# Kernel optimization log

Measured on AMD Instinct MI355X. Metric: run time of the kernel, lower is better.

The kernel has to match this reference:

```python
import jax, jax.numpy as jnp
import numpy as np

D_MODEL = 1024
N_HEADS = 16
D_K = D_MODEL // N_HEADS


def setup_inputs() -> dict:
    key = jax.random.key(0)
    ks = jax.random.split(key, 10)
    s = 1.0 / np.sqrt(D_MODEL)
    def lin(k):
        kw, kb = jax.random.split(k)
        W = jax.random.uniform(kw, (D_MODEL, D_MODEL), jnp.float32, -s, s)
        b = jax.random.uniform(kb, (D_MODEL,), jnp.float32, -s, s)
        return W, b
    Wq, bq = lin(ks[0])
    Wk, bk = lin(ks[1])
    Wv, bv = lin(ks[2])
    Wo, bo = lin(ks[3])
    x = jax.random.normal(ks[4], (2, 2048, D_MODEL), jnp.float32)
    gamma = jnp.ones((D_MODEL,), jnp.float32)
    beta = jnp.zeros((D_MODEL,), jnp.float32)
    return {"x": x, "Wq": Wq, "bq": bq, "Wk": Wk, "bk": bk,
            "Wv": Wv, "bv": bv, "Wo": Wo, "bo": bo,
            "gamma": gamma, "beta": beta}


def _mha(x, Wq, bq, Wk, bk, Wv, bv, Wo, bo, gamma, beta):
    B, S, _ = x.shape
    residual = x
    # Linear uses y = x @ W.T + b (torch nn.Linear convention)
    q = (x @ Wq.T + bq).reshape(B, S, N_HEADS, D_K).transpose(0, 2, 1, 3)
    k = (x @ Wk.T + bk).reshape(B, S, N_HEADS, D_K).transpose(0, 2, 1, 3)
    v = (x @ Wv.T + bv).reshape(B, S, N_HEADS, D_K).transpose(0, 2, 1, 3)
    scores = jnp.einsum("bhqd,bhkd->bhqk", q, k) / jnp.sqrt(jnp.float32(D_K))
    attn = jax.nn.softmax(scores, axis=-1)
    out = jnp.einsum("bhqk,bhkd->bhqd", attn, v)
    out = out.transpose(0, 2, 1, 3).reshape(B, S, D_MODEL)
    out = out @ Wo.T + bo
    h = out + residual
    mu = jnp.mean(h, axis=-1, keepdims=True)
    var = jnp.var(h, axis=-1, keepdims=True)
    h = (h - mu) / jnp.sqrt(var + 1e-5) * gamma + beta
    return jnp.where(h >= 0, h, 0.01 * h)


def reference(x, Wq, bq, Wk, bk, Wv, bv, Wo, bo, gamma, beta):
    return _mha(x, Wq, bq, Wk, bk, Wv, bv, Wo, bo, gamma, beta)
```

## Files before the change

### kernel.cpp

```cpp
#include <hip/hip_runtime.h>

#define DM   1024
#define NH   16
#define DK   64
#define SEQ  2048
#define BATCH 2

typedef __attribute__((ext_vector_type(8))) short bf16x8;
typedef __attribute__((ext_vector_type(4))) float f32x4;
typedef __attribute__((ext_vector_type(16))) float f32x16;

__device__ __forceinline__ unsigned short f2bf(float f) {
    unsigned int u = __builtin_bit_cast(unsigned int, f);
    u += 0x7FFFu + ((u >> 16) & 1u);
    return (unsigned short)(u >> 16);
}

__global__ __launch_bounds__(256)
void cvt_kernel(const float* __restrict__ x,
                const float* __restrict__ wq, const float* __restrict__ wk,
                const float* __restrict__ wv, const float* __restrict__ wo,
                unsigned short* __restrict__ xb,
                unsigned short* __restrict__ wqkvb,
                unsigned short* __restrict__ wob)
{
    const int seg = blockIdx.y;
    const float* src;
    unsigned short* dst;
    int n;
    if (seg == 0)      { src = x;  dst = xb;                  n = 4 << 20; }
    else if (seg == 1) { src = wq; dst = wqkvb;               n = 1 << 20; }
    else if (seg == 2) { src = wk; dst = wqkvb + (1 << 20);   n = 1 << 20; }
    else if (seg == 3) { src = wv; dst = wqkvb + (2 << 20);   n = 1 << 20; }
    else               { src = wo; dst = wob;                 n = 1 << 20; }
    for (int i = (blockIdx.x * 256 + threadIdx.x) * 4; i < n; i += 1024 * 256 * 4) {
        const float4 v = *reinterpret_cast<const float4*>(&src[i]);
        ushort4 o;
        o.x = f2bf(v.x); o.y = f2bf(v.y); o.z = f2bf(v.z); o.w = f2bf(v.w);
        *reinterpret_cast<ushort4*>(&dst[i]) = o;
    }
}

template <int MODE, int BN>
__global__ __launch_bounds__(256)
void gemm2_kernel(const unsigned short* __restrict__ Ab,
                  const unsigned short* __restrict__ Wall,
                  const float* __restrict__ B0, const float* __restrict__ B1,
                  const float* __restrict__ B2,
                  unsigned short* __restrict__ q_ws,
                  unsigned short* __restrict__ k_ws,
                  unsigned short* __restrict__ vt_ws,
                  const float* __restrict__ resid,
                  float* __restrict__ h_ws)
{
    __shared__ unsigned short sA[128 * 32];
    __shared__ unsigned short sB[BN * 32];

    const int tid = threadIdx.x, lane = tid & 63, wid = tid >> 6;
    const int n0 = blockIdx.x * BN, m0 = blockIdx.y * 128;
    const int z  = (MODE == 0) ? blockIdx.z : 0;
    const unsigned short* W = Wall + (size_t)z * (1 << 20);
    const float* bias = (MODE == 0) ? (z == 0 ? B0 : (z == 1 ? B1 : B2)) : B0;

    const int g = lane >> 4, lq = lane & 15;
    const int wr = wid >> 1, wc = wid & 1;
    const int rA = lane >> 2;
    const int csh = (lane & 3) * 8;

    f32x4 acc[4][BN / 32] = {};

    for (int k0 = 0; k0 < DM; k0 += 32) {
        #pragma unroll
        for (int i = 0; i < 2; ++i) {
            const int c = wid * 2 + i;
            __builtin_amdgcn_global_load_lds(
                (const __attribute__((address_space(1))) unsigned int*)
                    &Ab[(size_t)(m0 + c * 16 + rA) * DM + k0 + csh],
                (__attribute__((address_space(3))) unsigned int*)&sA[c * 512],
                16, 0, 0);
        }
        #pragma unroll
        for (int i = 0; i < BN / 64; ++i) {
            const int c = wid * (BN / 64) + i;
            __builtin_amdgcn_global_load_lds(
                (const __attribute__((address_space(1))) unsigned int*)
                    &W[(size_t)(n0 + c * 16 + rA) * DM + k0 + csh],
                (__attribute__((address_space(3))) unsigned int*)&sB[c * 512],
                16, 0, 0);
        }
        __syncthreads();

        bf16x8 a[4], b[BN / 32];
        #pragma unroll
        for (int m = 0; m < 4; ++m)
            a[m] = *reinterpret_cast<const bf16x8*>(&sA[(wr * 64 + m * 16 + lq) * 32 + 8 * g]);
        #pragma unroll
        for (int n = 0; n < BN / 32; ++n)
            b[n] = *reinterpret_cast<const bf16x8*>(&sB[(wc * (BN / 2) + n * 16 + lq) * 32 + 8 * g]);
        #pragma unroll
        for (int m = 0; m < 4; ++m)
            #pragma unroll
            for (int n = 0; n < BN / 32; ++n)
                acc[m][n] = __builtin_amdgcn_mfma_f32_16x16x32_bf16(
                    a[m], b[n], acc[m][n], 0, 0, 0);
        __syncthreads();
    }

    #pragma unroll
    for (int m = 0; m < 4; ++m) {
        #pragma unroll
        for (int n = 0; n < BN / 32; ++n) {
            #pragma unroll
            for (int j = 0; j < 4; ++j) {
                const int row = m0 + wr * 64 + m * 16 + 4 * g + j;
                const int col = n0 + wc * (BN / 2) + n * 16 + lq;
                float v = acc[m][n][j] + bias[col];
                if constexpr (MODE == 0) {
                    const int b_ = row >> 11, s = row & (SEQ - 1);
                    const int hh = col >> 6,  d = col & (DK - 1);
                    if (z == 0)
                        q_ws[(((size_t)(b_ * NH + hh) * SEQ + s) << 6) + d] = f2bf(v * 0.18033688f);
                    else if (z == 1)
                        k_ws[(((size_t)(b_ * NH + hh) * SEQ + s) << 6) + d] = f2bf(v);
                    else
                        vt_ws[((size_t)(b_ * NH + hh) * DK + d) * SEQ + s] = f2bf(v);
                } else {
                    const size_t idx = (size_t)row * DM + col;
                    h_ws[idx] = v + resid[idx];
                }
            }
        }
    }
}

__global__ __launch_bounds__(512)
void attn_kernel(const unsigned short* __restrict__ q_ws,
                 const unsigned short* __restrict__ k_ws,
                 const unsigned short* __restrict__ vt_ws,
                 unsigned short* __restrict__ ao_ws)
{
    __shared__ unsigned short lds4[8][4096];

    const int tid = threadIdx.x;
    const int lane = tid & 63, wid = tid >> 6;
    const int s = wid >> 2, w4 = wid & 3;
    const int l31 = lane & 31, h = lane >> 5;

    const int bid  = blockIdx.x + 16 * blockIdx.y;
    const int xcd  = bid & 7, slot = bid >> 3;
    const int bh   = 4 * xcd + (slot >> 4);
    const int q0   = (slot & 15) * 128;
    const int q    = q0 + w4 * 32 + l31;

    const size_t qbase = ((size_t)bh * SEQ + q) * DK;
    bf16x8 qf[4];
    #pragma unroll
    for (int j = 0; j < 4; ++j)
        qf[j] = *reinterpret_cast<const bf16x8*>(&q_ws[qbase + j * 16 + h * 8]);

    const short one_bf = (short)0x3F80;
    const bf16x8 onesf = {one_bf, one_bf, one_bf, one_bf, one_bf, one_bf, one_bf, one_bf};

    const int l8 = lane >> 3, l7 = lane & 7;
    const int scol = 8 * (l7 ^ l8);
    const unsigned short* kp0 = &k_ws [((size_t)bh * SEQ + s * 1024 + w4 * 16 + l8) * DK + scol];
    const unsigned short* kp1 = kp0 + 8 * DK;
    const unsigned short* vp0 = &vt_ws[((size_t)bh * DK + w4 * 16 + l8) * SEQ + s * 1024 + scol];
    const unsigned short* vp1 = vp0 + 8 * SEQ;

    const int r7 = l31 & 7;
    const unsigned short* pK[4];
    const unsigned short* pV[4];
    #pragma unroll
    for (int j = 0; j < 4; ++j) {
        const int ck = 8 * (((j << 1) + h) ^ r7);
        pK[j] = &lds4[2 * s][l31 * 64 + ck];
        pV[j] = &lds4[4 + 2 * s][l31 * 64 + ck];
    }

    f32x16 oacc[2] = {};
    f32x16 lacc = {};

    const int dst0 = w4 * 2 * 512, dst1 = (w4 * 2 + 1) * 512;

    auto stage = [&](int b) {
        __builtin_amdgcn_global_load_lds(
            (const __attribute__((address_space(1))) unsigned int*)kp0,
            (__attribute__((address_space(3))) unsigned int*)&lds4[2 * s + b][dst0], 16, 0, 0);
        __builtin_amdgcn_global_load_lds(
            (const __attribute__((address_space(1))) unsigned int*)kp1,
            (__attribute__((address_space(3))) unsigned int*)&lds4[2 * s + b][dst1], 16, 0, 0);
        __builtin_amdgcn_global_load_lds(
            (const __attribute__((address_space(1))) unsigned int*)vp0,
            (__attribute__((address_space(3))) unsigned int*)&lds4[4 + 2 * s + b][dst0], 16, 0, 0);
        __builtin_amdgcn_global_load_lds(
            (const __attribute__((address_space(1))) unsigned int*)vp1,
            (__attribute__((address_space(3))) unsigned int*)&lds4[4 + 2 * s + b][dst1], 16, 0, 0);
        kp0 += 64 * DK; kp1 += 64 * DK;
        vp0 += 64;      vp1 += 64;
    };

    auto compute = [&](int OFF) {
        f32x16 st0 = {}, st1 = {};
        __builtin_amdgcn_s_setprio(1);
        #pragma unroll
        for (int j = 0; j < 4; ++j) {
            const bf16x8 k0 = *reinterpret_cast<const bf16x8*>(pK[j] + OFF);
            const bf16x8 k1 = *reinterpret_cast<const bf16x8*>(pK[j] + OFF + 2048);
            st0 = __builtin_amdgcn_mfma_f32_32x32x16_bf16(k0, qf[j], st0, 0, 0, 0);
            st1 = __builtin_amdgcn_mfma_f32_32x32x16_bf16(k1, qf[j], st1, 0, 0, 0);
        }
        __builtin_amdgcn_s_setprio(0);

        bf16x8 pb[4];
        #pragma unroll
        for (int ss = 0; ss < 2; ++ss) {
            #pragma unroll
            for (int jg = 0; jg < 2; ++jg) {
                const int rb = 8 * jg;
                float e0, e1, e2, e3, e4, e5, e6, e7;
                #define EXP2(dst, src) asm("v_exp_f32 %0, %1" : "=v"(dst) : "v"(src))
                if (ss == 0) {
                    EXP2(e0, st0[rb + 0]); EXP2(e1, st0[rb + 1]);
                    EXP2(e2, st0[rb + 2]); EXP2(e3, st0[rb + 3]);
                    EXP2(e4, st0[rb + 4]); EXP2(e5, st0[rb + 5]);
                    EXP2(e6, st0[rb + 6]); EXP2(e7, st0[rb + 7]);
                } else {
                    EXP2(e0, st1[rb + 0]); EXP2(e1, st1[rb + 1]);
                    EXP2(e2, st1[rb + 2]); EXP2(e3, st1[rb + 3]);
                    EXP2(e4, st1[rb + 4]); EXP2(e5, st1[rb + 5]);
                    EXP2(e6, st1[rb + 6]); EXP2(e7, st1[rb + 7]);
                }
                #undef EXP2
                unsigned int wA, wB, wC, wD;
                asm("v_cvt_pk_bf16_f32 %0, %1, %2" : "=v"(wA) : "v"(e0), "v"(e1));
                asm("v_cvt_pk_bf16_f32 %0, %1, %2" : "=v"(wB) : "v"(e2), "v"(e3));
                asm("v_cvt_pk_bf16_f32 %0, %1, %2" : "=v"(wC) : "v"(e4), "v"(e5));
                asm("v_cvt_pk_bf16_f32 %0, %1, %2" : "=v"(wD) : "v"(e6), "v"(e7));
                asm("v_permlane32_swap_b32 %0, %1" : "+v"(wA), "+v"(wC));
                asm("v_permlane32_swap_b32 %0, %1" : "+v"(wB), "+v"(wD));
                uint4 ww;
                ww.x = wA; ww.y = wB; ww.z = wC; ww.w = wD;
                pb[2 * ss + jg] = __builtin_bit_cast(bf16x8, ww);
            }
        }

        __builtin_amdgcn_s_setprio(1);
        #pragma unroll
        for (int jg = 0; jg < 4; ++jg)
            lacc = __builtin_amdgcn_mfma_f32_32x32x16_bf16(onesf, pb[jg], lacc, 0, 0, 0);
        #pragma unroll
        for (int dt = 0; dt < 2; ++dt)
            #pragma unroll
            for (int jg = 0; jg < 4; ++jg) {
                const bf16x8 vv = *reinterpret_cast<const bf16x8*>(pV[jg] + OFF + dt * 2048);
                oacc[dt] = __builtin_amdgcn_mfma_f32_32x32x16_bf16(vv, pb[jg], oacc[dt], 0, 0, 0);
            }
        __builtin_amdgcn_s_setprio(0);
    };

    stage(0);
    __syncthreads();
    #pragma unroll 1
    for (int tt = 0; tt < 8; ++tt) {
        stage(1);
        compute(0);
        __syncthreads();
        if (tt < 7) stage(0);
        compute(4096);
        __syncthreads();
    }

    float* fl = (float*)&lds4[0][0];
    if (s == 1) {
        float* p = fl + (size_t)(w4 * 64 + lane) * 33;
        #pragma unroll
        for (int dt = 0; dt < 2; ++dt)
            #pragma unroll
            for (int r = 0; r < 16; ++r) p[dt * 16 + r] = oacc[dt][r];
        p[32] = lacc[0];
    }
    __syncthreads();
    if (s == 0) {
        const float* p = fl + (size_t)(w4 * 64 + lane) * 33;
        #pragma unroll
        for (int dt = 0; dt < 2; ++dt)
            #pragma unroll
            for (int r = 0; r < 16; ++r) oacc[dt][r] += p[dt * 16 + r];
        const float rl = 1.0f / (lacc[0] + p[32]);

        const int b_ = bh >> 4, hh = bh & 15;
        unsigned short* aop = &ao_ws[(size_t)(b_ * SEQ + q) * DM + hh * 64];
        #pragma unroll
        for (int dt = 0; dt < 2; ++dt) {
            #pragma unroll
            for (int qd = 0; qd < 4; ++qd) {
                ushort4 o;
                o.x = f2bf(oacc[dt][4 * qd + 0] * rl);
                o.y = f2bf(oacc[dt][4 * qd + 1] * rl);
                o.z = f2bf(oacc[dt][4 * qd + 2] * rl);
                o.w = f2bf(oacc[dt][4 * qd + 3] * rl);
                *reinterpret_cast<ushort4*>(&aop[dt * 32 + 8 * qd + 4 * h]) = o;
            }
        }
    }
}

__global__ __launch_bounds__(256)
void ln_kernel(const float* __restrict__ h, const float* __restrict__ gamma,
               const float* __restrict__ beta, float* __restrict__ out)
{
    __shared__ float s1[4], s2[4];
    const int row = blockIdx.x, tid = threadIdx.x;
    const float4 v = reinterpret_cast<const float4*>(h + (size_t)row * DM)[tid];
    float sum = v.x + v.y + v.z + v.w;
    float sq  = v.x * v.x + v.y * v.y + v.z * v.z + v.w * v.w;
    #pragma unroll
    for (int mk = 1; mk <= 32; mk <<= 1) {
        sum += __shfl_xor(sum, mk);
        sq  += __shfl_xor(sq, mk);
    }
    if ((tid & 63) == 0) { s1[tid >> 6] = sum; s2[tid >> 6] = sq; }
    __syncthreads();
    sum = s1[0] + s1[1] + s1[2] + s1[3];
    sq  = s2[0] + s2[1] + s2[2] + s2[3];
    const float mu = sum * (1.f / DM);
    const float var = sq * (1.f / DM) - mu * mu;
    const float rstd = rsqrtf(var + 1e-5f);
    const float4 gv = reinterpret_cast<const float4*>(gamma)[tid];
    const float4 bv = reinterpret_cast<const float4*>(beta)[tid];
    float4 o;
    o.x = (v.x - mu) * rstd * gv.x + bv.x;
    o.y = (v.y - mu) * rstd * gv.y + bv.y;
    o.z = (v.z - mu) * rstd * gv.z + bv.z;
    o.w = (v.w - mu) * rstd * gv.w + bv.w;
    o.x = o.x >= 0.f ? o.x : 0.01f * o.x;
    o.y = o.y >= 0.f ? o.y : 0.01f * o.y;
    o.z = o.z >= 0.f ? o.z : 0.01f * o.z;
    o.w = o.w >= 0.f ? o.w : 0.01f * o.w;
    reinterpret_cast<float4*>(out + (size_t)row * DM)[tid] = o;
}

extern "C" void kernel_launch(void* const* d_in, const int* in_sizes, int n_in,
                              void* d_out, int out_size, void* d_ws, size_t ws_size,
                              hipStream_t stream)
{
    const float* x     = (const float*)d_in[0];
    const float* Wq    = (const float*)d_in[1];
    const float* bq    = (const float*)d_in[2];
    const float* Wk    = (const float*)d_in[3];
    const float* bk    = (const float*)d_in[4];
    const float* Wv    = (const float*)d_in[5];
    const float* bv    = (const float*)d_in[6];
    const float* Wo    = (const float*)d_in[7];
    const float* bo    = (const float*)d_in[8];
    const float* gamma = (const float*)d_in[9];
    const float* beta  = (const float*)d_in[10];

    char* ws = (char*)d_ws;
    unsigned short* q_ws   = (unsigned short*)(ws);
    unsigned short* k_ws   = (unsigned short*)(ws + (8u << 20));
    unsigned short* vt_ws  = (unsigned short*)(ws + (16u << 20));
    unsigned short* ao_ws  = (unsigned short*)(ws + (24u << 20));
    unsigned short* xb_ws  = (unsigned short*)(ws + (32u << 20));
    unsigned short* wqkv_b = (unsigned short*)(ws + (40u << 20));
    unsigned short* wo_b   = (unsigned short*)(ws + (46u << 20));
    float* h_ws = (float*)ws;

    const dim3 blk(256);
    cvt_kernel<<<dim3(1024, 5), blk, 0, stream>>>(
        x, Wq, Wk, Wv, Wo, xb_ws, wqkv_b, wo_b);
    gemm2_kernel<0, 128><<<dim3(8, 32, 3), blk, 0, stream>>>(
        xb_ws, wqkv_b, bq, bk, bv, q_ws, k_ws, vt_ws, nullptr, nullptr);
    attn_kernel<<<dim3(16, 32), dim3(512), 0, stream>>>(q_ws, k_ws, vt_ws, ao_ws);
    gemm2_kernel<1, 64><<<dim3(16, 32, 1), blk, 0, stream>>>(
        ao_ws, wo_b, bo, nullptr, nullptr, nullptr, nullptr, nullptr, x, h_ws);
    ln_kernel<<<dim3(4096), blk, 0, stream>>>(h_ws, gamma, beta, (float*)d_out);
}
```

Measured before the change: 123.5 us.

## Load K/V fragments directly from global memory instead of staging through LDS

The attention kernel no longer double-buffers K and V^T tiles into shared memory with global_load_lds and block barriers. Each wave now reads its MFMA operand fragments straight from global memory, relying on L2/cache reuse across the four waves that share a tile. LDS shrinks to a small combine buffer, and launch bounds ask for higher occupancy. This removes barrier stalls and LDS traffic, but every wave now issues redundant global loads with no explicit prefetch and depends on latency hiding through occupancy.

```diff
diff --git a/kernel.cpp b/kernel.cpp
--- a/kernel.cpp
+++ b/kernel.cpp
@@ -133,13 +133,13 @@
     }
 }
 
-__global__ __launch_bounds__(512)
+__global__ __launch_bounds__(512, 7)
 void attn_kernel(const unsigned short* __restrict__ q_ws,
                  const unsigned short* __restrict__ k_ws,
                  const unsigned short* __restrict__ vt_ws,
                  unsigned short* __restrict__ ao_ws)
 {
-    __shared__ unsigned short lds4[8][4096];
+    __shared__ float comb[8448];
 
     const int tid = threadIdx.x;
     const int lane = tid & 63, wid = tid >> 6;
@@ -161,52 +161,21 @@
     const short one_bf = (short)0x3F80;
     const bf16x8 onesf = {one_bf, one_bf, one_bf, one_bf, one_bf, one_bf, one_bf, one_bf};
 
-    const int l8 = lane >> 3, l7 = lane & 7;
-    const int scol = 8 * (l7 ^ l8);
-    const unsigned short* kp0 = &k_ws [((size_t)bh * SEQ + s * 1024 + w4 * 16 + l8) * DK + scol];
-    const unsigned short* kp1 = kp0 + 8 * DK;
-    const unsigned short* vp0 = &vt_ws[((size_t)bh * DK + w4 * 16 + l8) * SEQ + s * 1024 + scol];
-    const unsigned short* vp1 = vp0 + 8 * SEQ;
-
-    const int r7 = l31 & 7;
-    const unsigned short* pK[4];
-    const unsigned short* pV[4];
-    #pragma unroll
-    for (int j = 0; j < 4; ++j) {
-        const int ck = 8 * (((j << 1) + h) ^ r7);
-        pK[j] = &lds4[2 * s][l31 * 64 + ck];
-        pV[j] = &lds4[4 + 2 * s][l31 * 64 + ck];
-    }
+    const unsigned short* kp  = &k_ws [((size_t)bh * SEQ + s * 1024 + l31) * DK + 8 * h];
+    const unsigned short* vp0 = &vt_ws[((size_t)bh * DK  + l31) * SEQ + s * 1024 + 8 * h];
+    const unsigned short* vp1 = vp0 + (size_t)32 * SEQ;
 
     f32x16 oacc[2] = {};
     f32x16 lacc = {};
 
-    const int dst0 = w4 * 2 * 512, dst1 = (w4 * 2 + 1) * 512;
-
-    auto stage = [&](int b) {
-        __builtin_amdgcn_global_load_lds(
-            (const __attribute__((address_space(1))) unsigned int*)kp0,
-            (__attribute__((address_space(3))) unsigned int*)&lds4[2 * s + b][dst0], 16, 0, 0);
-        __builtin_amdgcn_global_load_lds(
-            (const __attribute__((address_space(1))) unsigned int*)kp1,
-            (__attribute__((address_space(3))) unsigned int*)&lds4[2 * s + b][dst1], 16, 0, 0);
-        __builtin_amdgcn_global_load_lds(
-            (const __attribute__((address_space(1))) unsigned int*)vp0,
-            (__attribute__((address_space(3))) unsigned int*)&lds4[4 + 2 * s + b][dst0], 16, 0, 0);
-        __builtin_amdgcn_global_load_lds(
-            (const __attribute__((address_space(1))) unsigned int*)vp1,
-            (__attribute__((address_space(3))) unsigned int*)&lds4[4 + 2 * s + b][dst1], 16, 0, 0);
-        kp0 += 64 * DK; kp1 += 64 * DK;
-        vp0 += 64;      vp1 += 64;
-    };
-
-    auto compute = [&](int OFF) {
+    #pragma unroll 1
+    for (int t = 0; t < 16; ++t) {
         f32x16 st0 = {}, st1 = {};
         __builtin_amdgcn_s_setprio(1);
         #pragma unroll
         for (int j = 0; j < 4; ++j) {
-            const bf16x8 k0 = *reinterpret_cast<const bf16x8*>(pK[j] + OFF);
-            const bf16x8 k1 = *reinterpret_cast<const bf16x8*>(pK[j] + OFF + 2048);
+            const bf16x8 k0 = *reinterpret_cast<const bf16x8*>(kp + j * 16);
+            const bf16x8 k1 = *reinterpret_cast<const bf16x8*>(kp + 32 * DK + j * 16);
             st0 = __builtin_amdgcn_mfma_f32_32x32x16_bf16(k0, qf[j], st0, 0, 0, 0);
             st1 = __builtin_amdgcn_mfma_f32_32x32x16_bf16(k1, qf[j], st1, 0, 0, 0);
         }
@@ -250,30 +219,24 @@
         for (int jg = 0; jg < 4; ++jg)
             lacc = __builtin_amdgcn_mfma_f32_32x32x16_bf16(onesf, pb[jg], lacc, 0, 0, 0);
         #pragma unroll
-        for (int dt = 0; dt < 2; ++dt)
-            #pragma unroll
-            for (int jg = 0; jg < 4; ++jg) {
-                const bf16x8 vv = *reinterpret_cast<const bf16x8*>(pV[jg] + OFF + dt * 2048);
-                oacc[dt] = __builtin_amdgcn_mfma_f32_32x32x16_bf16(vv, pb[jg], oacc[dt], 0, 0, 0);
-            }
+        for (int jg = 0; jg < 4; ++jg) {
+            const bf16x8 vv = *reinterpret_cast<const bf16x8*>(vp0 + jg * 16);
+            oacc[0] = __builtin_amdgcn_mfma_f32_32x32x16_bf16(vv, pb[jg], oacc[0], 0, 0, 0);
+        }
+        #pragma unroll
+        for (int jg = 0; jg < 4; ++jg) {
+            const bf16x8 vv = *reinterpret_cast<const bf16x8*>(vp1 + jg * 16);
+            oacc[1] = __builtin_amdgcn_mfma_f32_32x32x16_bf16(vv, pb[jg], oacc[1], 0, 0, 0);
+        }
         __builtin_amdgcn_s_setprio(0);
-    };
-
-    stage(0);
-    __syncthreads();
-    #pragma unroll 1
-    for (int tt = 0; tt < 8; ++tt) {
-        stage(1);
-        compute(0);
-        __syncthreads();
-        if (tt < 7) stage(0);
-        compute(4096);
-        __syncthreads();
-    }
-
-    float* fl = (float*)&lds4[0][0];
+
+        kp  += 64 * DK;
+        vp0 += 64;
+        vp1 += 64;
+    }
+
     if (s == 1) {
-        float* p = fl + (size_t)(w4 * 64 + lane) * 33;
+        float* p = comb + (size_t)(w4 * 64 + lane) * 33;
         #pragma unroll
         for (int dt = 0; dt < 2; ++dt)
             #pragma unroll
@@ -282,7 +245,7 @@
     }
     __syncthreads();
     if (s == 0) {
-        const float* p = fl + (size_t)(w4 * 64 + lane) * 33;
+        const float* p = comb + (size_t)(w4 * 64 + lane) * 33;
         #pragma unroll
         for (int dt = 0; dt < 2; ++dt)
             #pragma unroll
```

New measurement: 481.0 us. 290% more time.

## Split attention KV range across four wave groups and drop the ones-MFMA row sum

Applied to the files above, without the earlier changes.

The attention block grows from 512 to 1024 threads, so four wave groups each handle a quarter of the key sequence instead of two groups handling halves. Double buffering is removed: each group single-buffers K and V in LDS with a sync before and after compute. The softmax denominator is now accumulated as a scalar sum of the exponentials plus a permlane swap, replacing the extra MFMA against a ones vector. The partial outputs are combined through LDS in two phases. This adds parallelism and cuts matrix work, but gives up load/compute overlap and adds synchronisation and register pressure under the 1024-thread launch bound.

```diff
diff --git a/kernel.cpp b/kernel.cpp
--- a/kernel.cpp
+++ b/kernel.cpp
@@ -133,7 +133,7 @@
     }
 }
 
-__global__ __launch_bounds__(512)
+__global__ __launch_bounds__(1024)
 void attn_kernel(const unsigned short* __restrict__ q_ws,
                  const unsigned short* __restrict__ k_ws,
                  const unsigned short* __restrict__ vt_ws,
@@ -158,14 +158,11 @@
     for (int j = 0; j < 4; ++j)
         qf[j] = *reinterpret_cast<const bf16x8*>(&q_ws[qbase + j * 16 + h * 8]);
 
-    const short one_bf = (short)0x3F80;
-    const bf16x8 onesf = {one_bf, one_bf, one_bf, one_bf, one_bf, one_bf, one_bf, one_bf};
-
     const int l8 = lane >> 3, l7 = lane & 7;
     const int scol = 8 * (l7 ^ l8);
-    const unsigned short* kp0 = &k_ws [((size_t)bh * SEQ + s * 1024 + w4 * 16 + l8) * DK + scol];
+    const unsigned short* kp0 = &k_ws [((size_t)bh * SEQ + s * 512 + w4 * 16 + l8) * DK + scol];
     const unsigned short* kp1 = kp0 + 8 * DK;
-    const unsigned short* vp0 = &vt_ws[((size_t)bh * DK + w4 * 16 + l8) * SEQ + s * 1024 + scol];
+    const unsigned short* vp0 = &vt_ws[((size_t)bh * DK + w4 * 16 + l8) * SEQ + s * 512 + scol];
     const unsigned short* vp1 = vp0 + 8 * SEQ;
 
     const int r7 = l31 & 7;
@@ -175,38 +172,38 @@
     for (int j = 0; j < 4; ++j) {
         const int ck = 8 * (((j << 1) + h) ^ r7);
         pK[j] = &lds4[2 * s][l31 * 64 + ck];
-        pV[j] = &lds4[4 + 2 * s][l31 * 64 + ck];
+        pV[j] = &lds4[2 * s + 1][l31 * 64 + ck];
     }
 
     f32x16 oacc[2] = {};
-    f32x16 lacc = {};
+    float lsum = 0.f;
 
     const int dst0 = w4 * 2 * 512, dst1 = (w4 * 2 + 1) * 512;
 
-    auto stage = [&](int b) {
+    auto stage = [&]() {
         __builtin_amdgcn_global_load_lds(
             (const __attribute__((address_space(1))) unsigned int*)kp0,
-            (__attribute__((address_space(3))) unsigned int*)&lds4[2 * s + b][dst0], 16, 0, 0);
+            (__attribute__((address_space(3))) unsigned int*)&lds4[2 * s][dst0], 16, 0, 0);
         __builtin_amdgcn_global_load_lds(
             (const __attribute__((address_space(1))) unsigned int*)kp1,
-            (__attribute__((address_space(3))) unsigned int*)&lds4[2 * s + b][dst1], 16, 0, 0);
+            (__attribute__((address_space(3))) unsigned int*)&lds4[2 * s][dst1], 16, 0, 0);
         __builtin_amdgcn_global_load_lds(
             (const __attribute__((address_space(1))) unsigned int*)vp0,
-            (__attribute__((address_space(3))) unsigned int*)&lds4[4 + 2 * s + b][dst0], 16, 0, 0);
+            (__attribute__((address_space(3))) unsigned int*)&lds4[2 * s + 1][dst0], 16, 0, 0);
         __builtin_amdgcn_global_load_lds(
             (const __attribute__((address_space(1))) unsigned int*)vp1,
-            (__attribute__((address_space(3))) unsigned int*)&lds4[4 + 2 * s + b][dst1], 16, 0, 0);
+            (__attribute__((address_space(3))) unsigned int*)&lds4[2 * s + 1][dst1], 16, 0, 0);
         kp0 += 64 * DK; kp1 += 64 * DK;
         vp0 += 64;      vp1 += 64;
     };
 
-    auto compute = [&](int OFF) {
+    auto compute = [&]() {
         f32x16 st0 = {}, st1 = {};
         __builtin_amdgcn_s_setprio(1);
         #pragma unroll
         for (int j = 0; j < 4; ++j) {
-            const bf16x8 k0 = *reinterpret_cast<const bf16x8*>(pK[j] + OFF);
-            const bf16x8 k1 = *reinterpret_cast<const bf16x8*>(pK[j] + OFF + 2048);
+            const bf16x8 k0 = *reinterpret_cast<const bf16x8*>(pK[j]);
+            const bf16x8 k1 = *reinterpret_cast<const bf16x8*>(pK[j] + 2048);
             st0 = __builtin_amdgcn_mfma_f32_32x32x16_bf16(k0, qf[j], st0, 0, 0, 0);
             st1 = __builtin_amdgcn_mfma_f32_32x32x16_bf16(k1, qf[j], st1, 0, 0, 0);
         }
@@ -232,6 +229,7 @@
                     EXP2(e6, st1[rb + 6]); EXP2(e7, st1[rb + 7]);
                 }
                 #undef EXP2
+                lsum += ((e0 + e1) + (e2 + e3)) + ((e4 + e5) + (e6 + e7));
                 unsigned int wA, wB, wC, wD;
                 asm("v_cvt_pk_bf16_f32 %0, %1, %2" : "=v"(wA) : "v"(e0), "v"(e1));
                 asm("v_cvt_pk_bf16_f32 %0, %1, %2" : "=v"(wB) : "v"(e2), "v"(e3));
@@ -247,48 +245,65 @@
 
         __builtin_amdgcn_s_setprio(1);
         #pragma unroll
-        for (int jg = 0; jg < 4; ++jg)
-            lacc = __builtin_amdgcn_mfma_f32_32x32x16_bf16(onesf, pb[jg], lacc, 0, 0, 0);
-        #pragma unroll
         for (int dt = 0; dt < 2; ++dt)
             #pragma unroll
             for (int jg = 0; jg < 4; ++jg) {
-                const bf16x8 vv = *reinterpret_cast<const bf16x8*>(pV[jg] + OFF + dt * 2048);
+                const bf16x8 vv = *reinterpret_cast<const bf16x8*>(pV[jg] + dt * 2048);
                 oacc[dt] = __builtin_amdgcn_mfma_f32_32x32x16_bf16(vv, pb[jg], oacc[dt], 0, 0, 0);
             }
         __builtin_amdgcn_s_setprio(0);
     };
 
-    stage(0);
-    __syncthreads();
     #pragma unroll 1
-    for (int tt = 0; tt < 8; ++tt) {
-        stage(1);
-        compute(0);
-        __syncthreads();
-        if (tt < 7) stage(0);
-        compute(4096);
-        __syncthreads();
-    }
+    for (int t = 0; t < 8; ++t) {
+        stage();
+        __syncthreads();
+        compute();
+        __syncthreads();
+    }
+
+    unsigned int la = __builtin_bit_cast(unsigned int, lsum);
+    unsigned int lb = la;
+    asm("v_permlane32_swap_b32 %0, %1" : "+v"(la), "+v"(lb));
+    float ltot = lsum + __builtin_bit_cast(float, h ? lb : la);
 
     float* fl = (float*)&lds4[0][0];
-    if (s == 1) {
-        float* p = fl + (size_t)(w4 * 64 + lane) * 33;
-        #pragma unroll
-        for (int dt = 0; dt < 2; ++dt)
-            #pragma unroll
-            for (int r = 0; r < 16; ++r) p[dt * 16 + r] = oacc[dt][r];
-        p[32] = lacc[0];
-    }
-    __syncthreads();
+    {
+        if (s > 0) {
+            float* p = fl + (size_t)((s - 1) * 256 + w4 * 64 + lane) * 17;
+            #pragma unroll
+            for (int r = 0; r < 16; ++r) p[r] = oacc[0][r];
+            p[16] = ltot;
+        }
+        __syncthreads();
+        if (s == 0) {
+            #pragma unroll
+            for (int ss2 = 0; ss2 < 3; ++ss2) {
+                const float* p = fl + (size_t)(ss2 * 256 + w4 * 64 + lane) * 17;
+                #pragma unroll
+                for (int r = 0; r < 16; ++r) oacc[0][r] += p[r];
+                ltot += p[16];
+            }
+        }
+        __syncthreads();
+        if (s > 0) {
+            float* p = fl + (size_t)((s - 1) * 256 + w4 * 64 + lane) * 17;
+            #pragma unroll
+            for (int r = 0; r < 16; ++r) p[r] = oacc[1][r];
+        }
+        __syncthreads();
+        if (s == 0) {
+            #pragma unroll
+            for (int ss2 = 0; ss2 < 3; ++ss2) {
+                const float* p = fl + (size_t)(ss2 * 256 + w4 * 64 + lane) * 17;
+                #pragma unroll
+                for (int r = 0; r < 16; ++r) oacc[1][r] += p[r];
+            }
+        }
+    }
+
     if (s == 0) {
-        const float* p = fl + (size_t)(w4 * 64 + lane) * 33;
-        #pragma unroll
-        for (int dt = 0; dt < 2; ++dt)
-            #pragma unroll
-            for (int r = 0; r < 16; ++r) oacc[dt][r] += p[dt * 16 + r];
-        const float rl = 1.0f / (lacc[0] + p[32]);
-
+        const float rl = 1.0f / ltot;
         const int b_ = bh >> 4, hh = bh & 15;
         unsigned short* aop = &ao_ws[(size_t)(b_ * SEQ + q) * DM + hh * 64];
         #pragma unroll
@@ -372,7 +387,7 @@
         x, Wq, Wk, Wv, Wo, xb_ws, wqkv_b, wo_b);
     gemm2_kernel<0, 128><<<dim3(8, 32, 3), blk, 0, stream>>>(
         xb_ws, wqkv_b, bq, bk, bv, q_ws, k_ws, vt_ws, nullptr, nullptr);
-    attn_kernel<<<dim3(16, 32), dim3(512), 0, stream>>>(q_ws, k_ws, vt_ws, ao_ws);
+    attn_kernel<<<dim3(16, 32), dim3(1024), 0, stream>>>(q_ws, k_ws, vt_ws, ao_ws);
     gemm2_kernel<1, 64><<<dim3(16, 32, 1), blk, 0, stream>>>(
         ao_ws, wo_b, bo, nullptr, nullptr, nullptr, nullptr, nullptr, x, h_ws);
     ln_kernel<<<dim3(4096), blk, 0, stream>>>(h_ws, gamma, beta, (float*)d_out);
```

Result: slower. 130.6 us (+5.8%).
